# Kernel tuning notes

Hardware: AMD Instinct MI355X
Metric: run time of the kernel (lower is better)

## Reference

```python
import jax, jax.numpy as jnp
import numpy as np

# dims from source: seq_len=784, d_in=2, d_hidden=512, d_out=2, n_layers=3; batch bumped 32->64
T, BS, D_IN, D_H, D_OUT, N_LAYERS = 784, 64, 2, 512, 2, 3


def _glorot(k, shape):
    fan_in, fan_out = shape[-2], shape[-1]
    std = jnp.sqrt(2.0 / (fan_in + fan_out)).astype(jnp.float32)
    return jax.random.normal(k, shape, jnp.float32) * std


def setup_inputs() -> dict:
    key = jax.random.key(0)
    ks = jax.random.split(key, 8)
    x = jax.random.normal(ks[0], (T, BS, D_IN), jnp.float32)
    W0 = _glorot(ks[1], (D_IN, D_H))
    b0 = jnp.zeros((D_H,), jnp.float32)
    # stable_init: uniform in [0.999, 1.001), one diagonal 'a' per layer
    A = jax.random.uniform(ks[2], (N_LAYERS, D_H), jnp.float32, 0.999, 1.001)
    B = _glorot(ks[3], (N_LAYERS, D_H, D_H))  # per-layer input matrix b
    C = _glorot(ks[4], (N_LAYERS, D_H, D_H))  # per-layer output matrix c
    Wf = _glorot(ks[5], (D_H, D_OUT))
    bf = jnp.zeros((D_OUT,), jnp.float32)
    return {"x": x, "W0": W0, "b0": b0, "A": A, "B": B, "C": C, "Wf": Wf, "bf": bf}


def _rnn_layer(x, a, b, c):
    # x: [T, BS, D], diagonal linear recurrence h_t = h_{t-1} * a + x_t @ b; y_t = h_t @ c
    u = jnp.einsum('tbi,ih->tbh', x, b)  # batched GEMM outside the scan

    def step(h, u_t):
        h = h * a + u_t
        return h, h

    h0 = jnp.zeros(u.shape[1:], u.dtype)  # [BS, D_H]
    _, hs = jax.lax.scan(step, h0, u)     # hs: [T, BS, D_H]
    return jnp.einsum('tbh,ho->tbo', hs, c)


def reference(x, W0, b0, A, B, C, Wf, bf):
    # initial Dense + relu
    h = jax.nn.relu(x @ W0 + b0)
    # stacked unidirectional RNN layers, relu after each
    for l in range(A.shape[0]):
        h = jax.nn.relu(_rnn_layer(h, A[l], B[l], C[l]))
    # final Dense (no residual)
    return h @ Wf + bf
```

## Files before the change

### kernel.cpp

```cpp
#include <hip/hip_runtime.h>
#include <hip/hip_bf16.h>

typedef _Float16 f16;
typedef f16 f16x8 __attribute__((ext_vector_type(8)));
typedef float f32x4 __attribute__((ext_vector_type(4)));

#define T_LEN 784
#define BATCH 64
#define DH 512
#define NCH (BATCH*DH)
#define M_ROWS (T_LEN*BATCH)
#define NCHUNK 16
#define CLEN 49

#define ACT_SCALE (1.0f/256.0f)
#define ACT_INV   256.0f

#define GLL16(g, s)                                                             \
    __builtin_amdgcn_global_load_lds(                                           \
        (const __attribute__((address_space(1))) void*)(g),                     \
        (__attribute__((address_space(3))) void*)(s), 16, 0, 0)

#define VMCNT(n) asm volatile("s_waitcnt vmcnt(" #n ")" ::: "memory")

__global__ void prep_weights(const float* __restrict__ B, const float* __restrict__ C,
                             f16* __restrict__ Bt, f16* __restrict__ Ct) {
    __shared__ float tile[32][33];
    int z = blockIdx.z;
    const float* src = (z < 3) ? (B + (size_t)z * DH * DH) : (C + (size_t)(z - 3) * DH * DH);
    f16* dst = (z < 3) ? (Bt + (size_t)z * DH * DH) : (Ct + (size_t)(z - 3) * DH * DH);
    int tx = threadIdx.x, ty = threadIdx.y;
    int nb = blockIdx.x * 32, kb = blockIdx.y * 32;
#pragma unroll
    for (int i = 0; i < 4; i++) {
        int k = ty + i * 8;
        tile[k][tx] = src[(size_t)(kb + k) * DH + nb + tx];
    }
    __syncthreads();
#pragma unroll
    for (int i = 0; i < 4; i++) {
        int n = ty + i * 8;
        dst[(size_t)(nb + n) * DH + kb + tx] = (f16)tile[tx][n];
    }
}

__global__ void dense0_kernel(const float* __restrict__ x, const float* __restrict__ W0,
                              const float* __restrict__ b0, f16* __restrict__ H) {
    int tid = blockIdx.x * 256 + threadIdx.x;
    int m = tid >> 6;
    int hb = (tid & 63) * 8;
    float x0 = x[(size_t)m * 2], x1 = x[(size_t)m * 2 + 1];
    f32x4 wa0 = *(const f32x4*)(W0 + hb);
    f32x4 wa1 = *(const f32x4*)(W0 + hb + 4);
    f32x4 wb0 = *(const f32x4*)(W0 + DH + hb);
    f32x4 wb1 = *(const f32x4*)(W0 + DH + hb + 4);
    f32x4 c0 = *(const f32x4*)(b0 + hb);
    f32x4 c1 = *(const f32x4*)(b0 + hb + 4);
    f16x8 o;
#pragma unroll
    for (int j = 0; j < 4; j++) {
        float v = fmaxf(fmaf(x0, wa0[j], fmaf(x1, wb0[j], c0[j])), 0.f) * ACT_SCALE;
        o[j] = (f16)v;
    }
#pragma unroll
    for (int j = 0; j < 4; j++) {
        float v = fmaxf(fmaf(x0, wa1[j], fmaf(x1, wb1[j], c1[j])), 0.f) * ACT_SCALE;
        o[4 + j] = (f16)v;
    }
    *(f16x8*)(H + (size_t)m * DH + hb) = o;
}

template <int RELU>
__global__ __launch_bounds__(256) void gemm_k(const f16* __restrict__ A,
                                              const f16* __restrict__ Bt,
                                              f16* __restrict__ Out) {
    __shared__ __align__(16) f16 As[3][128 * 32];
    __shared__ __align__(16) f16 Bs[3][128 * 32];
    const int tid = threadIdx.x;
    const int lane = tid & 63;
    const int wave = tid >> 6;
    const int wr = wave >> 1, wc = wave & 1;
    const size_t mb = (size_t)blockIdx.x * 128;
    const int nb = blockIdx.y * 128;

    const int rl = lane >> 2, sl = lane & 3;
    const int ssl = sl ^ ((rl >> 1) & 3);
    const int rowS0 = wave * 16 + rl;
    const int rowS1 = 64 + wave * 16 + rl;
    const f16* gA0 = A + (mb + rowS0) * DH + ssl * 8;
    const f16* gA1 = A + (mb + rowS1) * DH + ssl * 8;
    const f16* gB0 = Bt + (size_t)(nb + rowS0) * DH + ssl * 8;
    const f16* gB1 = Bt + (size_t)(nb + rowS1) * DH + ssl * 8;
    const int ldsOff0 = (wave * 16) * 32;
    const int ldsOff1 = (64 + wave * 16) * 32;

    const int rA = lane & 15, kq = lane >> 4;
    const int fsl = kq ^ ((rA >> 1) & 3);
    int offA[4], offB[4];
#pragma unroll
    for (int i = 0; i < 4; i++) offA[i] = (wr * 64 + i * 16 + rA) * 32 + fsl * 8;
#pragma unroll
    for (int j = 0; j < 4; j++) offB[j] = (wc * 64 + j * 16 + rA) * 32 + fsl * 8;

    f32x4 acc[4][4] = {};

#define STAGE(b, kt)                        \
    do {                                    \
        GLL16(gA0 + (kt), &As[b][ldsOff0]); \
        GLL16(gA1 + (kt), &As[b][ldsOff1]); \
        GLL16(gB0 + (kt), &Bs[b][ldsOff0]); \
        GLL16(gB1 + (kt), &Bs[b][ldsOff1]); \
    } while (0)

#define COMPUTE(b)                                                                              \
    do {                                                                                        \
        f16x8 af[4], bg[4];                                                                     \
        _Pragma("unroll") for (int i = 0; i < 4; i++) af[i] = *(const f16x8*)&As[b][offA[i]];   \
        _Pragma("unroll") for (int j = 0; j < 4; j++) bg[j] = *(const f16x8*)&Bs[b][offB[j]];   \
        _Pragma("unroll") for (int i = 0; i < 4; i++)                                           \
        _Pragma("unroll") for (int j = 0; j < 4; j++)                                           \
            acc[i][j] = __builtin_amdgcn_mfma_f32_16x16x32_f16(af[i], bg[j], acc[i][j], 0, 0, 0); \
    } while (0)

    STAGE(0, 0);
    STAGE(1, 32);

#pragma unroll
    for (int t = 0; t < 15; ++t) {
        VMCNT(4);
        __builtin_amdgcn_s_barrier();
        if (t < 14) STAGE((t + 2) % 3, (t + 2) * 32);
        COMPUTE(t % 3);
    }
    VMCNT(0);
    __builtin_amdgcn_s_barrier();
    COMPUTE(0);
#undef STAGE
#undef COMPUTE

    const int crow = (lane >> 4) * 4;
    const int ccol = lane & 15;
#pragma unroll
    for (int i = 0; i < 4; i++)
#pragma unroll
        for (int j = 0; j < 4; j++) {
#pragma unroll
            for (int r = 0; r < 4; r++) {
                size_t row = mb + wr * 64 + i * 16 + crow + r;
                int col = nb + wc * 64 + j * 16 + ccol;
                float v = acc[i][j][r];
                if (RELU) v = fmaxf(v, 0.f);
                Out[row * DH + col] = (f16)v;
            }
        }
}

__global__ void scan_pass1(const f16* __restrict__ U, const float* __restrict__ Al,
                           float* __restrict__ finals) {
    int tid = blockIdx.x * 256 + threadIdx.x;
    int ch = tid & (NCH - 1);
    int c = tid >> 15;
    float a = Al[ch & (DH - 1)];
    const f16* p = U + (size_t)(c * CLEN) * NCH + ch;
    float h = 0.f;
#pragma unroll
    for (int i = 0; i < CLEN; i++) h = fmaf(h, a, (float)p[(size_t)i * NCH]);
    finals[(size_t)c * NCH + ch] = h;
}

__global__ void scan_pass2(const float* __restrict__ finals, const float* __restrict__ Al,
                           float* __restrict__ carries) {
    int ch = blockIdx.x * 256 + threadIdx.x;
    float a = Al[ch & (DH - 1)];
    float a49 = 1.f;
#pragma unroll
    for (int i = 0; i < CLEN; i++) a49 *= a;
    float carry = 0.f;
#pragma unroll
    for (int c = 0; c < NCHUNK; c++) {
        carries[(size_t)c * NCH + ch] = carry;
        carry = fmaf(carry, a49, finals[(size_t)c * NCH + ch]);
    }
}

__global__ void scan_pass3(f16* __restrict__ U, const float* __restrict__ Al,
                           const float* __restrict__ carries) {
    int tid = blockIdx.x * 256 + threadIdx.x;
    int ch = tid & (NCH - 1);
    int c = tid >> 15;
    float a = Al[ch & (DH - 1)];
    f16* p = U + (size_t)(c * CLEN) * NCH + ch;
    float h = carries[(size_t)c * NCH + ch];
#pragma unroll
    for (int i = 0; i < CLEN; i++) {
        h = fmaf(h, a, (float)p[(size_t)i * NCH]);
        p[(size_t)i * NCH] = (f16)h;
    }
}

__global__ void final_dense(const f16* __restrict__ H, const float* __restrict__ Wf,
                            const float* __restrict__ bf_, float* __restrict__ out) {
    __shared__ float WfS[DH * 2];
    for (int i = threadIdx.x; i < DH * 2; i += 256) WfS[i] = Wf[i];
    __syncthreads();
    int wave = threadIdx.x >> 6, lane = threadIdx.x & 63;
    size_t m = (size_t)blockIdx.x * 4 + wave;
    f16x8 v = *(const f16x8*)(H + m * DH + lane * 8);
    float d0 = 0.f, d1 = 0.f;
#pragma unroll
    for (int j = 0; j < 8; j++) {
        float hv = (float)v[j];
        int h = lane * 8 + j;
        d0 = fmaf(hv, WfS[h * 2], d0);
        d1 = fmaf(hv, WfS[h * 2 + 1], d1);
    }
#pragma unroll
    for (int off = 32; off; off >>= 1) {
        d0 += __shfl_down(d0, off);
        d1 += __shfl_down(d1, off);
    }
    if (lane == 0) {
        out[m * 2] = fmaf(d0, ACT_INV, bf_[0]);
        out[m * 2 + 1] = fmaf(d1, ACT_INV, bf_[1]);
    }
}

extern "C" void kernel_launch(void* const* d_in, const int* in_sizes, int n_in,
                              void* d_out, int out_size, void* d_ws, size_t ws_size,
                              hipStream_t stream) {
    (void)in_sizes; (void)n_in; (void)out_size; (void)ws_size;
    const float* x   = (const float*)d_in[0];
    const float* W0  = (const float*)d_in[1];
    const float* b0  = (const float*)d_in[2];
    const float* A   = (const float*)d_in[3];
    const float* Bw  = (const float*)d_in[4];
    const float* Cw  = (const float*)d_in[5];
    const float* Wf  = (const float*)d_in[6];
    const float* bfv = (const float*)d_in[7];
    float* out = (float*)d_out;

    char* ws = (char*)d_ws;
    size_t off = 0;
    auto alloc = [&](size_t bytes) {
        void* p = ws + off;
        off += (bytes + 255) & ~(size_t)255;
        return p;
    };
    f16* Bt = (f16*)alloc((size_t)3 * DH * DH * 2);
    f16* Ct = (f16*)alloc((size_t)3 * DH * DH * 2);
    f16* P  = (f16*)alloc((size_t)M_ROWS * DH * 2);
    f16* Q  = (f16*)alloc((size_t)M_ROWS * DH * 2);
    float* finals  = (float*)alloc((size_t)NCH * NCHUNK * 4);
    float* carries = (float*)alloc((size_t)NCH * NCHUNK * 4);

    dim3 b256(256);
    prep_weights<<<dim3(16, 16, 6), dim3(32, 8), 0, stream>>>(Bw, Cw, Bt, Ct);
    dense0_kernel<<<M_ROWS * 64 / 256, b256, 0, stream>>>(x, W0, b0, P);
    for (int l = 0; l < 3; l++) {
        const float* Al = A + l * DH;
        gemm_k<0><<<dim3(M_ROWS / 128, 4), b256, 0, stream>>>(P, Bt + (size_t)l * DH * DH, Q);
        scan_pass1<<<NCH * NCHUNK / 256, b256, 0, stream>>>(Q, Al, finals);
        scan_pass2<<<NCH / 256, b256, 0, stream>>>(finals, Al, carries);
        scan_pass3<<<NCH * NCHUNK / 256, b256, 0, stream>>>(Q, Al, carries);
        gemm_k<1><<<dim3(M_ROWS / 128, 4), b256, 0, stream>>>(Q, Ct + (size_t)l * DH * DH, P);
    }
    final_dense<<<M_ROWS / 4, b256, 0, stream>>>(P, Wf, bfv, out);
}
```

Measured before the change: 365.8 us.

## Use 8-wave GEMM blocks and swap MFMA operands for vectorized stores

The GEMM block grows from 4 to 8 waves. Each wave now computes a 64x32 sub-tile instead of 64x64 and issues half as many global-to-LDS loads per stage. The MFMA operands are swapped so each lane holds four consecutive output columns, which turns the scalar f16 epilogue stores into 8-byte vector stores. This trades fewer accumulator registers and more waves per CU for latency hiding, against more LDS fragment reads per output and more barrier participants.

```diff
diff --git a/kernel.cpp b/kernel.cpp
--- a/kernel.cpp
+++ b/kernel.cpp
@@ -2,6 +2,7 @@
 #include <hip/hip_bf16.h>
 
 typedef _Float16 f16;
+typedef f16 f16x4 __attribute__((ext_vector_type(4)));
 typedef f16 f16x8 __attribute__((ext_vector_type(8)));
 typedef float f32x4 __attribute__((ext_vector_type(4)));
 
@@ -71,7 +72,7 @@
 }
 
 template <int RELU>
-__global__ __launch_bounds__(256) void gemm_k(const f16* __restrict__ A,
+__global__ __launch_bounds__(512) void gemm_k(const f16* __restrict__ A,
                                               const f16* __restrict__ Bt,
                                               f16* __restrict__ Out) {
     __shared__ __align__(16) f16 As[3][128 * 32];
@@ -79,47 +80,42 @@
     const int tid = threadIdx.x;
     const int lane = tid & 63;
     const int wave = tid >> 6;
-    const int wr = wave >> 1, wc = wave & 1;
+    const int wr = wave >> 2;
+    const int wc = wave & 3;
     const size_t mb = (size_t)blockIdx.x * 128;
     const int nb = blockIdx.y * 128;
 
     const int rl = lane >> 2, sl = lane & 3;
     const int ssl = sl ^ ((rl >> 1) & 3);
-    const int rowS0 = wave * 16 + rl;
-    const int rowS1 = 64 + wave * 16 + rl;
-    const f16* gA0 = A + (mb + rowS0) * DH + ssl * 8;
-    const f16* gA1 = A + (mb + rowS1) * DH + ssl * 8;
-    const f16* gB0 = Bt + (size_t)(nb + rowS0) * DH + ssl * 8;
-    const f16* gB1 = Bt + (size_t)(nb + rowS1) * DH + ssl * 8;
-    const int ldsOff0 = (wave * 16) * 32;
-    const int ldsOff1 = (64 + wave * 16) * 32;
+    const int rowS = wave * 16 + rl;
+    const f16* gA = A + (mb + rowS) * DH + ssl * 8;
+    const f16* gB = Bt + (size_t)(nb + rowS) * DH + ssl * 8;
+    const int ldsOff = (wave * 16) * 32;
 
     const int rA = lane & 15, kq = lane >> 4;
     const int fsl = kq ^ ((rA >> 1) & 3);
-    int offA[4], offB[4];
+    int offA[4], offB[2];
 #pragma unroll
     for (int i = 0; i < 4; i++) offA[i] = (wr * 64 + i * 16 + rA) * 32 + fsl * 8;
 #pragma unroll
-    for (int j = 0; j < 4; j++) offB[j] = (wc * 64 + j * 16 + rA) * 32 + fsl * 8;
-
-    f32x4 acc[4][4] = {};
-
-#define STAGE(b, kt)                        \
-    do {                                    \
-        GLL16(gA0 + (kt), &As[b][ldsOff0]); \
-        GLL16(gA1 + (kt), &As[b][ldsOff1]); \
-        GLL16(gB0 + (kt), &Bs[b][ldsOff0]); \
-        GLL16(gB1 + (kt), &Bs[b][ldsOff1]); \
+    for (int j = 0; j < 2; j++) offB[j] = (wc * 32 + j * 16 + rA) * 32 + fsl * 8;
+
+    f32x4 acc[4][2] = {};
+
+#define STAGE(b, kt)                       \
+    do {                                   \
+        GLL16(gA + (kt), &As[b][ldsOff]);  \
+        GLL16(gB + (kt), &Bs[b][ldsOff]);  \
     } while (0)
 
 #define COMPUTE(b)                                                                              \
     do {                                                                                        \
-        f16x8 af[4], bg[4];                                                                     \
+        f16x8 af[4], bg[2];                                                                     \
         _Pragma("unroll") for (int i = 0; i < 4; i++) af[i] = *(const f16x8*)&As[b][offA[i]];   \
-        _Pragma("unroll") for (int j = 0; j < 4; j++) bg[j] = *(const f16x8*)&Bs[b][offB[j]];   \
+        _Pragma("unroll") for (int j = 0; j < 2; j++) bg[j] = *(const f16x8*)&Bs[b][offB[j]];   \
         _Pragma("unroll") for (int i = 0; i < 4; i++)                                           \
-        _Pragma("unroll") for (int j = 0; j < 4; j++)                                           \
-            acc[i][j] = __builtin_amdgcn_mfma_f32_16x16x32_f16(af[i], bg[j], acc[i][j], 0, 0, 0); \
+        _Pragma("unroll") for (int j = 0; j < 2; j++)                                           \
+            acc[i][j] = __builtin_amdgcn_mfma_f32_16x16x32_f16(bg[j], af[i], acc[i][j], 0, 0, 0); \
     } while (0)
 
     STAGE(0, 0);
@@ -127,7 +123,7 @@
 
 #pragma unroll
     for (int t = 0; t < 15; ++t) {
-        VMCNT(4);
+        VMCNT(2);
         __builtin_amdgcn_s_barrier();
         if (t < 14) STAGE((t + 2) % 3, (t + 2) * 32);
         COMPUTE(t % 3);
@@ -138,21 +134,24 @@
 #undef STAGE
 #undef COMPUTE
 
-    const int crow = (lane >> 4) * 4;
-    const int ccol = lane & 15;
-#pragma unroll
-    for (int i = 0; i < 4; i++)
-#pragma unroll
-        for (int j = 0; j < 4; j++) {
+    const int erow = lane & 15;
+    const int ecq = (lane >> 4) * 4;
+#pragma unroll
+    for (int i = 0; i < 4; i++) {
+        size_t row = mb + wr * 64 + i * 16 + erow;
+#pragma unroll
+        for (int j = 0; j < 2; j++) {
+            int col = nb + wc * 32 + j * 16 + ecq;
+            f16x4 o;
 #pragma unroll
             for (int r = 0; r < 4; r++) {
-                size_t row = mb + wr * 64 + i * 16 + crow + r;
-                int col = nb + wc * 64 + j * 16 + ccol;
                 float v = acc[i][j][r];
                 if (RELU) v = fmaxf(v, 0.f);
-                Out[row * DH + col] = (f16)v;
+                o[r] = (f16)v;
             }
+            *(f16x4*)(Out + row * DH + col) = o;
         }
+    }
 }
 
 __global__ void scan_pass1(const f16* __restrict__ U, const float* __restrict__ Al,
@@ -254,15 +253,16 @@
     float* carries = (float*)alloc((size_t)NCH * NCHUNK * 4);
 
     dim3 b256(256);
+    dim3 b512(512);
     prep_weights<<<dim3(16, 16, 6), dim3(32, 8), 0, stream>>>(Bw, Cw, Bt, Ct);
     dense0_kernel<<<M_ROWS * 64 / 256, b256, 0, stream>>>(x, W0, b0, P);
     for (int l = 0; l < 3; l++) {
         const float* Al = A + l * DH;
-        gemm_k<0><<<dim3(M_ROWS / 128, 4), b256, 0, stream>>>(P, Bt + (size_t)l * DH * DH, Q);
+        gemm_k<0><<<dim3(M_ROWS / 128, 4), b512, 0, stream>>>(P, Bt + (size_t)l * DH * DH, Q);
         scan_pass1<<<NCH * NCHUNK / 256, b256, 0, stream>>>(Q, Al, finals);
         scan_pass2<<<NCH / 256, b256, 0, stream>>>(finals, Al, carries);
         scan_pass3<<<NCH * NCHUNK / 256, b256, 0, stream>>>(Q, Al, carries);
-        gemm_k<1><<<dim3(M_ROWS / 128, 4), b256, 0, stream>>>(Q, Ct + (size_t)l * DH * DH, P);
+        gemm_k<1><<<dim3(M_ROWS / 128, 4), b512, 0, stream>>>(Q, Ct + (size_t)l * DH * DH, P);
     }
     final_dense<<<M_ROWS / 4, b256, 0, stream>>>(P, Wf, bfv, out);
 }
```

After: 432.6 us. +18.3%, slower.
